# Kernel optimization log

Measured on AMD Instinct MI355X. Metric: run time of the kernel, lower is better.

## Reference

```python
import jax, jax.numpy as jnp
import numpy as np

B, S, D_MODEL, H, D_KV = 16, 512, 768, 12, 64
EPS = 1e-6
ROPE_THETA = 10000.0


def rms_norm(x, w, eps=EPS):
    var = jnp.mean(jnp.square(x.astype(jnp.float32)), axis=-1, keepdims=True)
    return w * (x * jax.lax.rsqrt(var + eps))


def rotate_half(x):
    x1, x2 = jnp.split(x, 2, axis=-1)
    return jnp.concatenate([-x2, x1], axis=-1)


def build_rope(position_ids, inv_freq):
    # position_ids: [B,S] int; inv_freq: [d_kv/2]
    freqs = position_ids[:, :, None].astype(jnp.float32) * inv_freq[None, None, :]  # [B,S,d/2]
    emb = jnp.concatenate([freqs, freqs], axis=-1)  # [B,S,d_kv]
    return jnp.cos(emb), jnp.sin(emb)


def shape_heads(x, n_heads, d_kv):
    b, s, _ = x.shape
    return x.reshape(b, s, n_heads, d_kv).transpose(0, 2, 1, 3)  # [b,h,s,d]


def attend(h, norm_w, wq, wk, wv, wo, mask, cos=None, sin=None):
    # h: [b,s,d_model]; mask: [b,h,s,s] additive
    normed = rms_norm(h, norm_w)
    q = shape_heads(normed @ wq.T, H, D_KV)
    k = shape_heads(normed @ wk.T, H, D_KV)
    v = shape_heads(normed @ wv.T, H, D_KV)
    if cos is not None:
        c = cos[:, None, :, :]
        s = sin[:, None, :, :]
        q = q * c + rotate_half(q) * s
        k = k * c + rotate_half(k) * s
    # NOTE: kernel has no 1/sqrt(d) scaling
    scores = jnp.einsum('bhqd,bhkd->bhqk', q, k) + mask
    p = jax.nn.softmax(scores, axis=-1)
    out = jnp.einsum('bhqk,bhkd->bhqd', p, v)
    b, _, s, _ = out.shape
    out = out.transpose(0, 2, 1, 3).reshape(b, s, H * D_KV)
    return h + out @ wo.T


def setup_inputs() -> dict:
    key = jax.random.key(0)
    ks = jax.random.split(key, 12)
    scale = 1.0 / np.sqrt(D_MODEL)
    inp = {
        'hidden_states': jax.random.normal(ks[0], (B, S, D_MODEL), dtype=jnp.float32),
        'position_ids': jnp.broadcast_to(jnp.arange(S, dtype=jnp.int32)[None, :], (B, S)),
        'attention_mask': jnp.broadcast_to(
            jnp.where(jnp.arange(S)[None, :] <= jnp.arange(S)[:, None], 0.0, -1e9).astype(jnp.float32),
            (B, H, S, S)) + 0.0,
        'group_time_mask': jnp.zeros((S, H, B, B), dtype=jnp.float32),
        't_q': jax.random.normal(ks[1], (H * D_KV, D_MODEL), dtype=jnp.float32) * scale,
        't_k': jax.random.normal(ks[2], (H * D_KV, D_MODEL), dtype=jnp.float32) * scale,
        't_v': jax.random.normal(ks[3], (H * D_KV, D_MODEL), dtype=jnp.float32) * scale,
        't_o': jax.random.normal(ks[4], (D_MODEL, H * D_KV), dtype=jnp.float32) * scale,
        't_norm_w': jnp.ones((D_MODEL,), dtype=jnp.float32),
        'g_q': jax.random.normal(ks[5], (H * D_KV, D_MODEL), dtype=jnp.float32) * scale,
        'g_k': jax.random.normal(ks[6], (H * D_KV, D_MODEL), dtype=jnp.float32) * scale,
        'g_v': jax.random.normal(ks[7], (H * D_KV, D_MODEL), dtype=jnp.float32) * scale,
        'g_o': jax.random.normal(ks[8], (D_MODEL, H * D_KV), dtype=jnp.float32) * scale,
        'g_norm_w': jnp.ones((D_MODEL,), dtype=jnp.float32),
        'inv_freq': (1.0 / ROPE_THETA ** (jnp.arange(0, D_KV, 2, dtype=jnp.float32) / D_KV)),
    }
    return inp


def reference(hidden_states, position_ids, attention_mask, group_time_mask,
              t_q, t_k, t_v, t_o, t_norm_w,
              g_q, g_k, g_v, g_o, g_norm_w, inv_freq):
    cos, sin = build_rope(position_ids, inv_freq)
    h = attend(hidden_states, t_norm_w, t_q, t_k, t_v, t_o, attention_mask, cos, sin)
    h = h.transpose(1, 0, 2)  # [S,B,D]: group attention attends across groups
    h = attend(h, g_norm_w, g_q, g_k, g_v, g_o, group_time_mask)
    return h.transpose(1, 0, 2)
```

## Files before the change

### kernel.cpp

```cpp
#include <hip/hip_runtime.h>

#define DM   768
#define QKVN 2304
#define SQ   512
#define NB   16
#define NH   12

typedef unsigned short u16;
typedef _Float16 h16;
typedef _Float16 h16x8 __attribute__((ext_vector_type(8)));
typedef float f32x4 __attribute__((ext_vector_type(4)));

__device__ __forceinline__ u16 f2h(float f) {
  h16 h = (h16)f;
  return __builtin_bit_cast(u16, h);
}
__device__ __forceinline__ float h2f(u16 u) {
  return (float)__builtin_bit_cast(h16, u);
}
__device__ __forceinline__ void gload_lds16(const void* g, void* l) {
  __builtin_amdgcn_global_load_lds((__attribute__((address_space(1))) void*)(g),
                                   (__attribute__((address_space(3))) void*)(l), 16, 0, 0);
}

struct WPtrs { const float* s[8]; u16* d[8]; };
__global__ __launch_bounds__(256) void prep_k(WPtrs P, const float* __restrict__ invf,
                                              float* __restrict__ tab,
                                              const float* __restrict__ x, const float* __restrict__ nw,
                                              u16* __restrict__ normed) {
  const int bid = blockIdx.x, tid = threadIdx.x;
  if (bid < 4608) {
    int w = bid / 576;
    int i = ((bid % 576) * 256 + tid) * 4;
    float4 v = *reinterpret_cast<const float4*>(P.s[w] + i);
    ushort4 o;
    o.x = f2h(v.x); o.y = f2h(v.y); o.z = f2h(v.z); o.w = f2h(v.w);
    *reinterpret_cast<ushort4*>(P.d[w] + i) = o;
  } else if (bid < 4672) {
    int i = (bid - 4608) * 256 + tid;
    int pos = i >> 5, j = i & 31;
    float a = (float)pos * invf[j];
    float s, c;
    sincosf(a, &s, &c);
    tab[i * 2] = c; tab[i * 2 + 1] = s;
  } else {
    int wv = tid >> 6, lane = tid & 63;
    size_t t = (size_t)(bid - 4672) * 4 + wv;
    const float* row = x + t * DM;
    float4 v[3];
    float ss = 0.f;
#pragma unroll
    for (int i = 0; i < 3; i++) {
      v[i] = *reinterpret_cast<const float4*>(row + (lane + 64 * i) * 4);
      ss += v[i].x * v[i].x + v[i].y * v[i].y + v[i].z * v[i].z + v[i].w * v[i].w;
    }
#pragma unroll
    for (int d = 1; d < 64; d <<= 1) ss += __shfl_xor(ss, d);
    float rs = rsqrtf(ss * (1.0f / 768.f) + 1e-6f);
    u16* orow = normed + t * DM;
#pragma unroll
    for (int i = 0; i < 3; i++) {
      int c = (lane + 64 * i) * 4;
      float4 wv4 = *reinterpret_cast<const float4*>(nw + c);
      ushort4 o;
      o.x = f2h(v[i].x * rs * wv4.x);
      o.y = f2h(v[i].y * rs * wv4.y);
      o.z = f2h(v[i].z * rs * wv4.z);
      o.w = f2h(v[i].w * rs * wv4.w);
      *reinterpret_cast<ushort4*>(orow + c) = o;
    }
  }
}

__global__ __launch_bounds__(256) void rms_k(const float* __restrict__ x, const float* __restrict__ w,
                                             u16* __restrict__ out) {
  int wv = threadIdx.x >> 6, lane = threadIdx.x & 63;
  size_t t = (size_t)blockIdx.x * 4 + wv;
  const float* row = x + t * DM;
  float4 v[3];
  float ss = 0.f;
#pragma unroll
  for (int i = 0; i < 3; i++) {
    v[i] = *reinterpret_cast<const float4*>(row + (lane + 64 * i) * 4);
    ss += v[i].x * v[i].x + v[i].y * v[i].y + v[i].z * v[i].z + v[i].w * v[i].w;
  }
#pragma unroll
  for (int d = 1; d < 64; d <<= 1) ss += __shfl_xor(ss, d);
  float rs = rsqrtf(ss * (1.0f / 768.f) + 1e-6f);
  u16* orow = out + t * DM;
#pragma unroll
  for (int i = 0; i < 3; i++) {
    int c = (lane + 64 * i) * 4;
    float4 wv4 = *reinterpret_cast<const float4*>(w + c);
    ushort4 o;
    o.x = f2h(v[i].x * rs * wv4.x);
    o.y = f2h(v[i].y * rs * wv4.y);
    o.z = f2h(v[i].z * rs * wv4.z);
    o.w = f2h(v[i].w * rs * wv4.w);
    *reinterpret_cast<ushort4*>(orow + c) = o;
  }
}

template <bool RESID, bool ROPE, int PERM>
__global__ __launch_bounds__(256, 2) void gemm_k(const u16* __restrict__ A, const u16* __restrict__ W, int N,
                                              u16* __restrict__ Cb, float* __restrict__ Cf,
                                              const float* __restrict__ resid,
                                              const int* __restrict__ pids, const float* __restrict__ tab) {
  __shared__ __align__(16) char L[4 * 16384];
  const int tid = threadIdx.x, w = tid >> 6, lane = tid & 63;
  const int wr = w >> 1, wc = w & 1;
  const int nbn = gridDim.y;
  int nf = blockIdx.y * gridDim.x + blockIdx.x;
  int nwg = gridDim.x * nbn;
  int swv = (nf & 7) * (nwg >> 3) + (nf >> 3);
  const int bm = swv / nbn;
  const int bnb = swv % nbn;
  const int l15 = lane & 15, l4 = lane >> 4;
  f32x4 acc[4][4] = {};

  const int r0 = tid >> 2, k40 = tid & 3;
  const int k4s = k40 ^ ((r0 >> 1) & 3);
  const size_t aA0 = (size_t)(bm * 128 + r0) * 1536 + k4s * 16;
  const size_t aA1 = (size_t)(bm * 128 + r0 + 64) * 1536 + k4s * 16;
  const size_t aB0 = (size_t)(bnb * 128 + r0) * 1536 + k4s * 16;
  const size_t aB1 = (size_t)(bnb * 128 + r0 + 64) * 1536 + k4s * 16;
  const int dc0 = tid * 16, dc1 = dc0 + 4096;
  const char* Ab = (const char*)A;
  const char* Wb = (const char*)W;

#define STAGE(T64, Q) do { \
    gload_lds16(Ab + aA0 + (T64), L + (Q) * 16384 + dc0); \
    gload_lds16(Ab + aA1 + (T64), L + (Q) * 16384 + dc1); \
    gload_lds16(Wb + aB0 + (T64), L + (Q) * 16384 + 8192 + dc0); \
    gload_lds16(Wb + aB1 + (T64), L + (Q) * 16384 + 8192 + dc1); \
  } while (0)

  int obA[4], obB[4];
#pragma unroll
  for (int i = 0; i < 4; i++) {
    int rowA = wr * 64 + i * 16 + l15;
    obA[i] = rowA * 64 + ((l4 ^ ((rowA >> 1) & 3)) * 16);
    int rowB = wc * 64 + i * 16 + l15;
    obB[i] = 8192 + rowB * 64 + ((l4 ^ ((rowB >> 1) & 3)) * 16);
  }

  STAGE(0, 0); STAGE(64, 1); STAGE(128, 2);
  asm volatile("s_waitcnt vmcnt(8)" ::: "memory");
  __builtin_amdgcn_sched_barrier(0);
  __builtin_amdgcn_s_barrier();
  __builtin_amdgcn_sched_barrier(0);

#pragma unroll
  for (int to = 0; to < 6; ++to) {
#pragma unroll
    for (int ti = 0; ti < 4; ++ti) {
      const int t = to * 4 + ti;
      const int tn = (t + 3 < 24) ? (t + 3) : 23;
      STAGE(tn * 64, (t + 3) & 3);
      const char* bq = L + (t & 3) * 16384;
      h16x8 am[4], bn[4];
#pragma unroll
      for (int i = 0; i < 4; i++) am[i] = *reinterpret_cast<const h16x8*>(bq + obA[i]);
#pragma unroll
      for (int j = 0; j < 4; j++) bn[j] = *reinterpret_cast<const h16x8*>(bq + obB[j]);
      __builtin_amdgcn_s_setprio(1);
#pragma unroll
      for (int i = 0; i < 4; i++)
#pragma unroll
        for (int j = 0; j < 4; j++)
          acc[i][j] = __builtin_amdgcn_mfma_f32_16x16x32_f16(am[i], bn[j], acc[i][j], 0, 0, 0);
      __builtin_amdgcn_s_setprio(0);
      asm volatile("s_waitcnt vmcnt(8)" ::: "memory");
      __builtin_amdgcn_sched_barrier(0);
      __builtin_amdgcn_s_barrier();
      __builtin_amdgcn_sched_barrier(0);
    }
  }
#undef STAGE
  asm volatile("s_waitcnt vmcnt(0)" ::: "memory");

  if (ROPE && bnb < 12) {
#pragma unroll
    for (int i = 0; i < 4; i++) {
      int row0 = bm * 128 + wr * 64 + i * 16 + l4 * 4;
#pragma unroll
      for (int r = 0; r < 4; r++) {
        int pos = pids[row0 + r];
        const float* tb = tab + pos * 64;
#pragma unroll
        for (int j = 0; j < 2; j++) {
          float2 cs = *reinterpret_cast<const float2*>(tb + 2 * (j * 16 + l15));
          float x1 = acc[i][j][r], x2 = acc[i][j + 2][r];
          acc[i][j][r]     = x1 * cs.x - x2 * cs.y;
          acc[i][j + 2][r] = x2 * cs.x + x1 * cs.y;
        }
      }
    }
  }
#pragma unroll
  for (int i = 0; i < 4; i++) {
    int row0 = bm * 128 + wr * 64 + i * 16 + l4 * 4;
#pragma unroll
    for (int j = 0; j < 4; j++) {
      int col = bnb * 128 + wc * 64 + j * 16 + l15;
#pragma unroll
      for (int r = 0; r < 4; r++) {
        int rr = row0 + r;
        int orow = (PERM == 0) ? rr : (PERM == 1) ? ((rr & 511) * 16 + (rr >> 9))
                                                  : ((rr & 15) * 512 + (rr >> 4));
        size_t idx = (size_t)orow * N + col;
        float v = acc[i][j][r];
        if (RESID) Cf[idx] = v + resid[idx];
        else Cb[idx] = f2h(v);
      }
    }
  }
}

__global__ __launch_bounds__(256) void vtrans_k(const u16* __restrict__ qkv, u16* __restrict__ vt) {
  __shared__ u16 T[64][72];
  const int st = blockIdx.x, bh = blockIdx.y;
  const int b = bh / NH, h = bh % NH;
  const int t = threadIdx.x;
  {
    int s = t >> 2, d0 = (t & 3) * 16;
    const u16* src = qkv + ((size_t)(b * SQ + st * 64 + s)) * QKVN + 2 * DM + h * 64 + d0;
    ushort4 a0 = *reinterpret_cast<const ushort4*>(src + 0);
    ushort4 a1 = *reinterpret_cast<const ushort4*>(src + 4);
    ushort4 a2 = *reinterpret_cast<const ushort4*>(src + 8);
    ushort4 a3 = *reinterpret_cast<const ushort4*>(src + 12);
    *reinterpret_cast<ushort4*>(&T[s][d0 + 0])  = a0;
    *reinterpret_cast<ushort4*>(&T[s][d0 + 4])  = a1;
    *reinterpret_cast<ushort4*>(&T[s][d0 + 8])  = a2;
    *reinterpret_cast<ushort4*>(&T[s][d0 + 12]) = a3;
  }
  __syncthreads();
  {
    int d = t >> 2, k0 = (t & 3) * 16;
    u16* dst = vt + ((size_t)bh * 64 + d) * SQ + st * 64 + k0;
    ushort4 o[4];
#pragma unroll
    for (int i = 0; i < 16; i++) ((u16*)o)[i] = T[k0 + i][d];
#pragma unroll
    for (int i = 0; i < 4; i++) *reinterpret_cast<ushort4*>(dst + i * 4) = o[i];
  }
}

__global__ __launch_bounds__(256) void attn1_k(const u16* __restrict__ qkv, const u16* __restrict__ vt,
                                               u16* __restrict__ O) {
  __shared__ __align__(16) char L[2][32768];
  __shared__ __align__(16) char Pl[4][4096];
  const int qt = blockIdx.x;
  const int bh = blockIdx.y;
  const int b = bh / NH, h = bh % NH;
  const int tid = threadIdx.x, w = tid >> 6, lane = tid & 63;
  const int l15 = lane & 15, l4 = lane >> 4;
  const size_t qoff = ((size_t)(b * SQ + qt * 64 + w * 16 + l15)) * QKVN + h * 64;
  h16x8 qf[2];
  qf[0] = *reinterpret_cast<const h16x8*>(qkv + qoff + 8 * l4);
  qf[1] = *reinterpret_cast<const h16x8*>(qkv + qoff + 32 + 8 * l4);
  f32x4 acco[4] = {};
  float mrun[4] = {-3e38f, -3e38f, -3e38f, -3e38f};
  float lrun[4] = {0.f, 0.f, 0.f, 0.f};
  const int qrow = qt * 64 + w * 16 + l4 * 4;
  const int nkt = (qt >> 1) + 1;

  const u16* Kg = qkv + (size_t)b * SQ * QKVN + DM + h * 64;
  const int rK0 = tid >> 3;
  const size_t aK0 = (size_t)rK0 * QKVN + (size_t)(((tid & 7) ^ (rK0 & 7)) * 8);
  const u16* Vg = vt + (size_t)bh * 64 * SQ;
  const int dV0 = tid >> 4;
  const size_t aV0 = (size_t)dV0 * SQ + (size_t)(((tid & 15) ^ (dV0 & 15)) * 8);
  const int dst0 = tid * 16;

#define STAGE1(KT, BUF) do { \
    _Pragma("unroll") \
    for (int e = 0; e < 4; e++) \
      gload_lds16(Kg + aK0 + (size_t)e * (32 * QKVN) + (size_t)(KT) * (128 * QKVN), \
                  L[BUF] + dst0 + e * 4096); \
    _Pragma("unroll") \
    for (int e = 0; e < 4; e++) \
      gload_lds16(Vg + aV0 + e * (16 * SQ) + (KT) * 128, \
                  L[BUF] + 16384 + dst0 + e * 4096); \
  } while (0)

  STAGE1(0, 0);
  asm volatile("s_waitcnt vmcnt(0)" ::: "memory");
  __builtin_amdgcn_sched_barrier(0);
  __builtin_amdgcn_s_barrier();
  __builtin_amdgcn_sched_barrier(0);

  for (int kt = 0; kt < nkt; ++kt) {
    const int cur = kt & 1;
    if (kt + 1 < nkt) STAGE1(kt + 1, cur ^ 1);
    const char* Kb = L[cur];
    const char* Vb = L[cur] + 16384;
    f32x4 sc[8] = {};
    __builtin_amdgcn_s_setprio(1);
#pragma unroll
    for (int kk = 0; kk < 2; kk++) {
#pragma unroll
      for (int j = 0; j < 8; j++) {
        int row = j * 16 + l15;
        int off = row * 128 + (((kk * 4 + l4) ^ (row & 7)) * 16);
        h16x8 kf = *reinterpret_cast<const h16x8*>(Kb + off);
        sc[j] = __builtin_amdgcn_mfma_f32_16x16x32_f16(qf[kk], kf, sc[j], 0, 0, 0);
      }
    }
    __builtin_amdgcn_s_setprio(0);
    float pv[8][4];
#pragma unroll
    for (int j = 0; j < 8; j++)
#pragma unroll
      for (int r = 0; r < 4; r++) pv[j][r] = sc[j][r];
    if (kt == nkt - 1) {
#pragma unroll
      for (int r = 0; r < 4; r++) {
        int q = qrow + r;
#pragma unroll
        for (int j = 0; j < 8; j++) {
          int key = kt * 128 + j * 16 + l15;
          if (key > q) pv[j][r] = -1e30f;
        }
      }
    }
    float al[4];
#pragma unroll
    for (int r = 0; r < 4; r++) {
      float t0 = fmaxf(fmaxf(pv[0][r], pv[1][r]), fmaxf(pv[2][r], pv[3][r]));
      float t1 = fmaxf(fmaxf(pv[4][r], pv[5][r]), fmaxf(pv[6][r], pv[7][r]));
      float tm = fmaxf(t0, t1);
      tm = fmaxf(tm, __shfl_xor(tm, 1)); tm = fmaxf(tm, __shfl_xor(tm, 2));
      tm = fmaxf(tm, __shfl_xor(tm, 4)); tm = fmaxf(tm, __shfl_xor(tm, 8));
      float mn = fmaxf(mrun[r], tm);
      al[r] = __expf(mrun[r] - mn);
      mrun[r] = mn;
      float ts = 0.f;
#pragma unroll
      for (int j = 0; j < 8; j++) { float p = __expf(pv[j][r] - mn); pv[j][r] = p; ts += p; }
      ts += __shfl_xor(ts, 1); ts += __shfl_xor(ts, 2); ts += __shfl_xor(ts, 4); ts += __shfl_xor(ts, 8);
      lrun[r] = lrun[r] * al[r] + ts;
    }
#pragma unroll
    for (int j = 0; j < 4; j++)
#pragma unroll
      for (int r = 0; r < 4; r++) acco[j][r] *= al[r];
    char* pw = Pl[w];
#pragma unroll
    for (int r = 0; r < 4; r++) {
      int q = l4 * 4 + r;
#pragma unroll
      for (int j = 0; j < 8; j++) {
        int cw = j * 2 + (l15 >> 3);
        int byte = q * 256 + ((cw ^ (q & 15)) * 16) + (l15 & 7) * 2;
        *(u16*)(pw + byte) = f2h(pv[j][r]);
      }
    }
    asm volatile("s_waitcnt lgkmcnt(0)" ::: "memory");
    __builtin_amdgcn_sched_barrier(0);
    __builtin_amdgcn_s_setprio(1);
#pragma unroll
    for (int kk = 0; kk < 4; kk++) {
      h16x8 pa = *reinterpret_cast<const h16x8*>(pw + l15 * 256 + (((kk * 4 + l4) ^ l15) * 16));
#pragma unroll
      for (int j = 0; j < 4; j++) {
        int d = j * 16 + l15;
        int voff = d * 256 + (((kk * 4 + l4) ^ (d & 15)) * 16);
        h16x8 vf = *reinterpret_cast<const h16x8*>(Vb + voff);
        acco[j] = __builtin_amdgcn_mfma_f32_16x16x32_f16(pa, vf, acco[j], 0, 0, 0);
      }
    }
    __builtin_amdgcn_s_setprio(0);
    asm volatile("s_waitcnt vmcnt(0)" ::: "memory");
    __builtin_amdgcn_sched_barrier(0);
    __builtin_amdgcn_s_barrier();
    __builtin_amdgcn_sched_barrier(0);
  }
#undef STAGE1
#pragma unroll
  for (int r = 0; r < 4; r++) {
    float inv = 1.f / lrun[r];
    size_t orow = ((size_t)(b * SQ + qrow + r)) * DM + h * 64;
#pragma unroll
    for (int j = 0; j < 4; j++) O[orow + j * 16 + l15] = f2h(acco[j][r] * inv);
  }
}

__global__ __launch_bounds__(256) void attn2_k(const u16* __restrict__ qkv, const float* __restrict__ gmask,
                                               u16* __restrict__ O) {
  __shared__ float Pl[4][16][16];
  __shared__ float Vl[4][16][68];
  const int tid = threadIdx.x, w = tid >> 6, lane = tid & 63;
  const int idx = blockIdx.x * 4 + w;
  const int s = idx / NH, h = idx % NH;
  const int l15 = lane & 15, l4 = lane >> 4;
  const size_t base = ((size_t)(s * 16 + l15)) * QKVN + h * 64;
  h16x8 qf0 = *reinterpret_cast<const h16x8*>(qkv + base + 8 * l4);
  h16x8 qf1 = *reinterpret_cast<const h16x8*>(qkv + base + 32 + 8 * l4);
  h16x8 kf0 = *reinterpret_cast<const h16x8*>(qkv + base + DM + 8 * l4);
  h16x8 kf1 = *reinterpret_cast<const h16x8*>(qkv + base + DM + 32 + 8 * l4);
  f32x4 sc = {};
  sc = __builtin_amdgcn_mfma_f32_16x16x32_f16(qf0, kf0, sc, 0, 0, 0);
  sc = __builtin_amdgcn_mfma_f32_16x16x32_f16(qf1, kf1, sc, 0, 0, 0);
  {
    int key = lane >> 2, d0 = (lane & 3) * 16;
    const u16* vsrc = qkv + ((size_t)(s * 16 + key)) * QKVN + 2 * DM + h * 64 + d0;
#pragma unroll
    for (int i = 0; i < 16; i += 4) {
      ushort4 vv = *reinterpret_cast<const ushort4*>(vsrc + i);
      Vl[w][key][d0 + i + 0] = h2f(vv.x);
      Vl[w][key][d0 + i + 1] = h2f(vv.y);
      Vl[w][key][d0 + i + 2] = h2f(vv.z);
      Vl[w][key][d0 + i + 3] = h2f(vv.w);
    }
  }
  const float* gm = gmask + ((size_t)s * NH + h) * 256;
#pragma unroll
  for (int r = 0; r < 4; r++) {
    float v = sc[r] + gm[(l4 * 4 + r) * 16 + l15];
    float mx = v;
    mx = fmaxf(mx, __shfl_xor(mx, 1)); mx = fmaxf(mx, __shfl_xor(mx, 2));
    mx = fmaxf(mx, __shfl_xor(mx, 4)); mx = fmaxf(mx, __shfl_xor(mx, 8));
    float p = __expf(v - mx);
    float su = p;
    su += __shfl_xor(su, 1); su += __shfl_xor(su, 2); su += __shfl_xor(su, 4); su += __shfl_xor(su, 8);
    Pl[w][l4 * 4 + r][l15] = p / su;
  }
  asm volatile("s_waitcnt lgkmcnt(0)" ::: "memory");
  __builtin_amdgcn_sched_barrier(0);
  const int q = lane >> 2, d0 = (lane & 3) * 16;
  float o[16] = {};
#pragma unroll
  for (int key = 0; key < 16; key++) {
    float pp = Pl[w][q][key];
#pragma unroll
    for (int dd = 0; dd < 16; dd += 4) {
      float4 vv = *reinterpret_cast<const float4*>(&Vl[w][key][d0 + dd]);
      o[dd + 0] += pp * vv.x; o[dd + 1] += pp * vv.y; o[dd + 2] += pp * vv.z; o[dd + 3] += pp * vv.w;
    }
  }
  u16* orow = O + ((size_t)(s * 16 + q)) * DM + h * 64 + d0;
#pragma unroll
  for (int i = 0; i < 16; i += 4) {
    ushort4 ov;
    ov.x = f2h(o[i]); ov.y = f2h(o[i + 1]); ov.z = f2h(o[i + 2]); ov.w = f2h(o[i + 3]);
    *reinterpret_cast<ushort4*>(orow + i) = ov;
  }
}

extern "C" void kernel_launch(void* const* d_in, const int* in_sizes, int n_in,
                              void* d_out, int out_size, void* d_ws, size_t ws_size,
                              hipStream_t stream) {
  const float* hidden = (const float*)d_in[0];
  const int*   pids   = (const int*)d_in[1];
  const float* gmask  = (const float*)d_in[3];
  const float* tq = (const float*)d_in[4];
  const float* tk = (const float*)d_in[5];
  const float* tv = (const float*)d_in[6];
  const float* to_ = (const float*)d_in[7];
  const float* tnw = (const float*)d_in[8];
  const float* gq = (const float*)d_in[9];
  const float* gk = (const float*)d_in[10];
  const float* gv = (const float*)d_in[11];
  const float* go = (const float*)d_in[12];
  const float* gnw = (const float*)d_in[13];
  const float* invf = (const float*)d_in[14];
  float* out = (float*)d_out;
  char* ws = (char*)d_ws;

  u16*   wq1    = (u16*)(ws);
  u16*   wo1    = (u16*)(ws + 3538944);
  u16*   wq2    = (u16*)(ws + 4718592);
  u16*   wo2    = (u16*)(ws + 8257536);
  float* tab    = (float*)(ws + 9437184);
  u16*   normed = (u16*)(ws + 9568256);
  u16*   obuf   = (u16*)(ws + 22151168);
  float* h1     = (float*)(ws + 34734080);
  u16*   qkv    = (u16*)(ws + 59899904);
  u16*   vt     = (u16*)(ws + 97648640);

  const int WN = 768 * 768;
  WPtrs P;
  P.s[0] = tq;  P.d[0] = wq1;
  P.s[1] = tk;  P.d[1] = wq1 + WN;
  P.s[2] = tv;  P.d[2] = wq1 + 2 * WN;
  P.s[3] = to_; P.d[3] = wo1;
  P.s[4] = gq;  P.d[4] = wq2;
  P.s[5] = gk;  P.d[5] = wq2 + WN;
  P.s[6] = gv;  P.d[6] = wq2 + 2 * WN;
  P.s[7] = go;  P.d[7] = wo2;

  prep_k<<<6720, 256, 0, stream>>>(P, invf, tab, hidden, tnw, normed);
  gemm_k<false, true, 0><<<dim3(64, 18), 256, 0, stream>>>(normed, wq1, QKVN, qkv, nullptr, nullptr, pids, tab);
  vtrans_k<<<dim3(8, 192), 256, 0, stream>>>(qkv, vt);
  attn1_k<<<dim3(8, 192), 256, 0, stream>>>(qkv, vt, obuf);
  gemm_k<true, false, 0><<<dim3(64, 6), 256, 0, stream>>>(obuf, wo1, DM, nullptr, h1, hidden, nullptr, nullptr);

  rms_k<<<2048, 256, 0, stream>>>(h1, gnw, normed);
  gemm_k<false, false, 1><<<dim3(64, 18), 256, 0, stream>>>(normed, wq2, QKVN, qkv, nullptr, nullptr, nullptr, nullptr);
  attn2_k<<<1536, 256, 0, stream>>>(qkv, gmask, obuf);
  gemm_k<true, false, 2><<<dim3(64, 6), 256, 0, stream>>>(obuf, wo2, DM, nullptr, out, h1, nullptr, nullptr);
}
```

Measured before the change: 216.9 us.

## Fuse V transpose into QKV GEMM epilogue and store intermediate hidden in fp16

The QKV projection GEMM now writes the V columns directly in transposed [b,h,d,s] layout from its accumulators, which removes the separate vtrans kernel launch and its read/write pass over V. The intermediate residual h1 is stored as fp16 instead of fp32, halving its traffic in the out-projection epilogue, rms_k, and the final residual add. The transposed stores are 8-byte scattered writes with stride 512. Rounding h1 to fp16 adds precision loss to the residual path.

```diff
diff --git a/kernel.cpp b/kernel.cpp
--- a/kernel.cpp
+++ b/kernel.cpp
@@ -72,16 +72,17 @@
   }
 }
 
-__global__ __launch_bounds__(256) void rms_k(const float* __restrict__ x, const float* __restrict__ w,
+__global__ __launch_bounds__(256) void rms_k(const u16* __restrict__ x, const float* __restrict__ w,
                                              u16* __restrict__ out) {
   int wv = threadIdx.x >> 6, lane = threadIdx.x & 63;
   size_t t = (size_t)blockIdx.x * 4 + wv;
-  const float* row = x + t * DM;
+  const u16* row = x + t * DM;
   float4 v[3];
   float ss = 0.f;
 #pragma unroll
   for (int i = 0; i < 3; i++) {
-    v[i] = *reinterpret_cast<const float4*>(row + (lane + 64 * i) * 4);
+    ushort4 rw = *reinterpret_cast<const ushort4*>(row + (lane + 64 * i) * 4);
+    v[i].x = h2f(rw.x); v[i].y = h2f(rw.y); v[i].z = h2f(rw.z); v[i].w = h2f(rw.w);
     ss += v[i].x * v[i].x + v[i].y * v[i].y + v[i].z * v[i].z + v[i].w * v[i].w;
   }
 #pragma unroll
@@ -101,11 +102,11 @@
   }
 }
 
-template <bool RESID, bool ROPE, int PERM>
+template <int CMODE, bool ROPE, int PERM, bool VT>
 __global__ __launch_bounds__(256, 2) void gemm_k(const u16* __restrict__ A, const u16* __restrict__ W, int N,
-                                              u16* __restrict__ Cb, float* __restrict__ Cf,
-                                              const float* __restrict__ resid,
-                                              const int* __restrict__ pids, const float* __restrict__ tab) {
+                                              void* __restrict__ C, const void* __restrict__ resid,
+                                              const int* __restrict__ pids, const float* __restrict__ tab,
+                                              u16* __restrict__ vt) {
   __shared__ __align__(16) char L[4 * 16384];
   const int tid = threadIdx.x, w = tid >> 6, lane = tid & 63;
   const int wr = w >> 1, wc = w & 1;
@@ -179,6 +180,25 @@
 #undef STAGE
   asm volatile("s_waitcnt vmcnt(0)" ::: "memory");
 
+  if (VT && bnb >= 12) {
+#pragma unroll
+    for (int i = 0; i < 4; i++) {
+      int row0 = bm * 128 + wr * 64 + i * 16 + l4 * 4;
+      int b = row0 >> 9, s0 = row0 & 511;
+#pragma unroll
+      for (int j = 0; j < 4; j++) {
+        int vcol = bnb * 128 + wc * 64 + j * 16 + l15 - 1536;
+        int hh = vcol >> 6, dd = vcol & 63;
+        u16* dst = vt + (((size_t)(b * NH + hh) * 64 + dd) << 9) + s0;
+        ushort4 o;
+        o.x = f2h(acc[i][j][0]); o.y = f2h(acc[i][j][1]);
+        o.z = f2h(acc[i][j][2]); o.w = f2h(acc[i][j][3]);
+        *reinterpret_cast<ushort4*>(dst) = o;
+      }
+    }
+    return;
+  }
+
   if (ROPE && bnb < 12) {
 #pragma unroll
     for (int i = 0; i < 4; i++) {
@@ -210,39 +230,11 @@
                                                   : ((rr & 15) * 512 + (rr >> 4));
         size_t idx = (size_t)orow * N + col;
         float v = acc[i][j][r];
-        if (RESID) Cf[idx] = v + resid[idx];
-        else Cb[idx] = f2h(v);
-      }
-    }
-  }
-}
-
-__global__ __launch_bounds__(256) void vtrans_k(const u16* __restrict__ qkv, u16* __restrict__ vt) {
-  __shared__ u16 T[64][72];
-  const int st = blockIdx.x, bh = blockIdx.y;
-  const int b = bh / NH, h = bh % NH;
-  const int t = threadIdx.x;
-  {
-    int s = t >> 2, d0 = (t & 3) * 16;
-    const u16* src = qkv + ((size_t)(b * SQ + st * 64 + s)) * QKVN + 2 * DM + h * 64 + d0;
-    ushort4 a0 = *reinterpret_cast<const ushort4*>(src + 0);
-    ushort4 a1 = *reinterpret_cast<const ushort4*>(src + 4);
-    ushort4 a2 = *reinterpret_cast<const ushort4*>(src + 8);
-    ushort4 a3 = *reinterpret_cast<const ushort4*>(src + 12);
-    *reinterpret_cast<ushort4*>(&T[s][d0 + 0])  = a0;
-    *reinterpret_cast<ushort4*>(&T[s][d0 + 4])  = a1;
-    *reinterpret_cast<ushort4*>(&T[s][d0 + 8])  = a2;
-    *reinterpret_cast<ushort4*>(&T[s][d0 + 12]) = a3;
-  }
-  __syncthreads();
-  {
-    int d = t >> 2, k0 = (t & 3) * 16;
-    u16* dst = vt + ((size_t)bh * 64 + d) * SQ + st * 64 + k0;
-    ushort4 o[4];
-#pragma unroll
-    for (int i = 0; i < 16; i++) ((u16*)o)[i] = T[k0 + i][d];
-#pragma unroll
-    for (int i = 0; i < 4; i++) *reinterpret_cast<ushort4*>(dst + i * 4) = o[i];
+        if (CMODE == 0)      ((u16*)C)[idx] = f2h(v);
+        else if (CMODE == 1) ((u16*)C)[idx] = f2h(v + ((const float*)resid)[idx]);
+        else                 ((float*)C)[idx] = v + h2f(((const u16*)resid)[idx]);
+      }
+    }
   }
 }
 
@@ -475,7 +467,7 @@
   float* tab    = (float*)(ws + 9437184);
   u16*   normed = (u16*)(ws + 9568256);
   u16*   obuf   = (u16*)(ws + 22151168);
-  float* h1     = (float*)(ws + 34734080);
+  u16*   h1     = (u16*)(ws + 34734080);
   u16*   qkv    = (u16*)(ws + 59899904);
   u16*   vt     = (u16*)(ws + 97648640);
 
@@ -491,13 +483,12 @@
   P.s[7] = go;  P.d[7] = wo2;
 
   prep_k<<<6720, 256, 0, stream>>>(P, invf, tab, hidden, tnw, normed);
-  gemm_k<false, true, 0><<<dim3(64, 18), 256, 0, stream>>>(normed, wq1, QKVN, qkv, nullptr, nullptr, pids, tab);
-  vtrans_k<<<dim3(8, 192), 256, 0, stream>>>(qkv, vt);
+  gemm_k<0, true, 0, true><<<dim3(64, 18), 256, 0, stream>>>(normed, wq1, QKVN, qkv, nullptr, pids, tab, vt);
   attn1_k<<<dim3(8, 192), 256, 0, stream>>>(qkv, vt, obuf);
-  gemm_k<true, false, 0><<<dim3(64, 6), 256, 0, stream>>>(obuf, wo1, DM, nullptr, h1, hidden, nullptr, nullptr);
+  gemm_k<1, false, 0, false><<<dim3(64, 6), 256, 0, stream>>>(obuf, wo1, DM, h1, hidden, nullptr, nullptr, nullptr);
 
   rms_k<<<2048, 256, 0, stream>>>(h1, gnw, normed);
-  gemm_k<false, false, 1><<<dim3(64, 18), 256, 0, stream>>>(normed, wq2, QKVN, qkv, nullptr, nullptr, nullptr, nullptr);
+  gemm_k<0, false, 1, false><<<dim3(64, 18), 256, 0, stream>>>(normed, wq2, QKVN, qkv, nullptr, nullptr, nullptr, nullptr);
   attn2_k<<<1536, 256, 0, stream>>>(qkv, gmask, obuf);
-  gemm_k<true, false, 2><<<dim3(64, 6), 256, 0, stream>>>(obuf, wo2, DM, nullptr, out, h1, nullptr, nullptr);
-}
+  gemm_k<2, false, 2, false><<<dim3(64, 6), 256, 0, stream>>>(obuf, wo2, DM, out, h1, nullptr, nullptr, nullptr);
+}
```

New measurement: 208.7 us. 3.8% less time.
